# Kernel optimization log

Measured on AMD Instinct MI355X. Metric: run time of the kernel, lower is better.

## Reference

```python
import jax, jax.numpy as jnp
import numpy as np

V = 128          # vocab_size
S = 32           # sentence_size
E = 16           # embedding_size
M = 128          # memory_size
L = 128          # linear_output_size
B = 16
N = 127


def _position_encoding(sentence_size, embedding_size):
    enc = np.ones((embedding_size, sentence_size), dtype=np.float32)
    ls = sentence_size + 1
    le = embedding_size + 1
    for i in range(1, le):
        for j in range(1, ls):
            enc[i - 1, j - 1] = (i - (le - 1) / 2) * (j - (ls - 1) / 2)
    enc = 1 + 4 * enc / embedding_size / sentence_size
    return enc.T  # [S, E]


def setup_inputs() -> dict:
    key = jax.random.key(0)
    ks = jax.random.split(key, 12)
    node_fts = jax.random.randint(ks[0], (B, N, S), 0, V).astype(jnp.float32)
    edge_fts = jax.random.randint(ks[1], (B, N, N, S), 0, V).astype(jnp.float32)
    graph_fts = jax.random.randint(ks[2], (B, S), 0, V).astype(jnp.float32)
    adj_mat = jax.random.randint(ks[3], (B, N, N), 0, 2).astype(jnp.float32)
    hidden = jnp.zeros((B, N, E), jnp.float32)
    sc = 0.02
    query_biases = sc * jax.random.normal(ks[4], (V - 1, E), jnp.float32)
    stories_biases = sc * jax.random.normal(ks[5], (V - 1, E), jnp.float32)
    output_biases = sc * jax.random.normal(ks[6], (V - 1, E), jnp.float32)
    memory_contents = sc * jax.random.normal(ks[7], (M, E), jnp.float32)
    W_int = sc * jax.random.normal(ks[8], (E, E), jnp.float32)   # intermediate_linear (unused, num_hops=1)
    W_out = sc * jax.random.normal(ks[9], (E, L), jnp.float32)   # output_linear
    W_fin = sc * jax.random.normal(ks[10], (L, V), jnp.float32)  # final_linear
    enc = jnp.asarray(_position_encoding(S, E))
    return dict(node_fts=node_fts, edge_fts=edge_fts, graph_fts=graph_fts,
                adj_mat=adj_mat, hidden=hidden, enc=enc,
                query_biases=query_biases, stories_biases=stories_biases,
                output_biases=output_biases, memory_contents=memory_contents,
                W_int=W_int, W_out=W_out, W_fin=W_fin)


def reference(node_fts, edge_fts, graph_fts, adj_mat, hidden, enc,
              query_biases, stories_biases, output_biases, memory_contents,
              W_int, W_out, W_fin):
    del hidden
    b, n, s = node_fts.shape
    # [B, N+1, S]: nodes plus graph feature row
    naf = jnp.concatenate([node_fts, graph_fts[:, None, :]], axis=1)
    # mask edges then pad to [B, N+1, N+1, S]
    ef = edge_fts * adj_mat[..., None]
    ef = jnp.pad(ef, ((0, 0), (0, 1), (0, 1), (0, 0)))
    bt = b * (n + 1)
    queries = naf.reshape(bt, s)                 # [BT, S]
    stories = ef.reshape(bt, n + 1, s)           # [BT, M0, S], M0 = N+1

    nil = jnp.zeros((1, enc.shape[1]), queries.dtype)
    sb = jnp.concatenate([stories_biases, nil], axis=0)   # [V, E]
    qb = jnp.concatenate([query_biases, nil], axis=0)
    ob = jnp.concatenate([output_biases, nil], axis=0)

    sidx = jnp.maximum(stories.astype(jnp.int32), 0)       # clamp_min(0)
    qidx = jnp.maximum(queries.astype(jnp.int32), 0)

    # position-encoded weighted sums over the sentence axis
    mem = jnp.einsum('bmse,se->bme', sb[sidx], enc)        # [BT, M0, E]
    Cj = jnp.einsum('bmse,se->bme', ob[sidx], enc)         # [BT, M0, E]
    pad_m = memory_contents.shape[0] - (n + 1)
    mem = jnp.pad(mem, ((0, 0), (0, pad_m), (0, 0))) + memory_contents
    Cj = jnp.pad(Cj, ((0, 0), (0, pad_m), (0, 0)))
    u = jnp.einsum('bse,se->be', qb[qidx], enc)            # [BT, E]

    # num_hops = 1
    x = u
    probs = jax.nn.softmax(jnp.einsum('bme,be->bm', mem, x), axis=-1)
    o = jnp.einsum('bme,bm->be', Cj, probs)
    x = jax.nn.relu((x + o) @ W_out)                       # last hop -> output_linear + relu
    ret = x @ W_fin                                        # [BT, V]

    nxt = ret.reshape(b, n + 1, -1)
    return nxt[:, :-1, :] + nxt[:, -1:, :]                 # [B, N, V]
```

## Files before the change

kernel.cpp:

```cpp
#include <hip/hip_runtime.h>

#define Vn 128
#define Bn 16
#define Nn 127
#define BTn 2048
#define TRS 20

__device__ __forceinline__ unsigned rneb(float f) {
    unsigned u = __float_as_uint(f);
    return (u + 0x7fffu + ((u >> 16) & 1u)) >> 16;
}
__device__ __forceinline__ float encf(int s, float e7) {
    return fmaf(e7, (float)(s - 15) * 0.0078125f, 1.0f);
}

__global__ __launch_bounds__(256, 4) void memnet_main(
    const float* __restrict__ node_fts, const float* __restrict__ edge_fts,
    const float* __restrict__ graph_fts, const float* __restrict__ adjm,
    const float* __restrict__ qb, const float* __restrict__ sb,
    const float* __restrict__ ob, const float* __restrict__ mc,
    const float* __restrict__ wout, const float* __restrict__ wfin,
    float* __restrict__ ret)
{
    __shared__ __align__(16) unsigned tblL[128 * TRS];
    __shared__ unsigned idxw[8 * 128];
    __shared__ float cjT[16 * 129];
    __shared__ float scoresL[128];
    __shared__ float probsL[128];
    __shared__ float opart[128];
    __shared__ unsigned char actF[128];
    __shared__ __align__(16) float uL[16];
    __shared__ float uoL[16];
    __shared__ __align__(16) float cCL[16];
    __shared__ float xL[128];
    __shared__ float red[8];
    __shared__ float k0L;

    const int t = threadIdx.x;
    const int bt = blockIdx.x;
    const int b = bt >> 7;
    const int i = bt & 127;

    for (int c = t; c < 512; c += 256) {
        int r = c >> 2, q = c & 3;
        float4 s4 = make_float4(0.f, 0.f, 0.f, 0.f);
        float4 o4 = make_float4(0.f, 0.f, 0.f, 0.f);
        if (r < 127) {
            s4 = *(const float4*)&sb[r * 16 + q * 4];
            o4 = *(const float4*)&ob[r * 16 + q * 4];
        }
        uint4 pk;
        pk.x = (rneb(o4.x) << 16) | rneb(s4.x);
        pk.y = (rneb(o4.y) << 16) | rneb(s4.y);
        pk.z = (rneb(o4.z) << 16) | rneb(s4.z);
        pk.w = (rneb(o4.w) << 16) | rneb(s4.w);
        *(uint4*)&tblL[r * TRS + q * 4] = pk;
    }
    if (t < 128) {
        bool a = false;
        if (t < 127 && i < 127) a = (adjm[(b * 127 + i) * 127 + t] != 0.f);
        actF[t] = a ? 1 : 0;
    }
    for (int c = t; c < 1024; c += 256) {
        int m = c >> 3, q = c & 7;
        unsigned packed = 0u;
        if (i < 127 && m < 127) {
            float a = adjm[(b * 127 + i) * 127 + m];
            if (a != 0.f) {
                const float4 v = *(const float4*)&edge_fts[(size_t)(((b * 127 + i) * 127 + m)) * 32 + q * 4];
                packed = (unsigned)(int)v.x | ((unsigned)(int)v.y << 8)
                       | ((unsigned)(int)v.z << 16) | ((unsigned)(int)v.w << 24);
            }
        }
        idxw[q * 128 + m] = packed;
    }
    if (t < 16) {
        const float e7 = (float)(t - 7);
        float es = 0.f, ue = 0.f;
        for (int s = 0; s < 32; s++) {
            float ev = encf(s, e7);
            es += ev;
            float qv = (i < 127) ? node_fts[(b * 127 + i) * 32 + s] : graph_fts[b * 32 + s];
            int qi = (int)qv;
            if (qi < 0) qi = 0;
            float w = (qi < 127) ? qb[qi * 16 + t] : 0.f;
            ue = fmaf(w, ev, ue);
        }
        uL[t] = ue;
        cCL[t] = ob[t] * es;
        float kv = sb[t] * es * ue;
        kv += __shfl_xor(kv, 1); kv += __shfl_xor(kv, 2);
        kv += __shfl_xor(kv, 4); kv += __shfl_xor(kv, 8);
        if (t == 0) k0L = kv;
    }
    __syncthreads();

    const int eg4 = (t & 3) * 4;
    const int md = t >> 2;
    const int m0 = md;
    const int m1 = md + 64;
    const bool a0 = (actF[m0] != 0);
    const bool a1 = (actF[m1] != 0);
    const float ef0 = (float)(eg4 - 7), ef1 = (float)(eg4 - 6);
    const float ef2 = (float)(eg4 - 5), ef3 = (float)(eg4 - 4);

    float4 aM0 = make_float4(0.f, 0.f, 0.f, 0.f);
    float4 aM1 = make_float4(0.f, 0.f, 0.f, 0.f);
    float4 aC0 = make_float4(0.f, 0.f, 0.f, 0.f);
    float4 aC1 = make_float4(0.f, 0.f, 0.f, 0.f);

    if (a0) {
#pragma unroll
        for (int sq = 0; sq < 8; sq++) {
            unsigned w0 = idxw[sq * 128 + m0];
#pragma unroll
            for (int j = 0; j < 4; j++) {
                const int s = sq * 4 + j;
                int ix = (int)((w0 >> (8 * j)) & 0xFF);
                const uint4 pk = *(const uint4*)&tblL[ix * TRS + eg4];
                float e0 = encf(s, ef0), e1 = encf(s, ef1);
                float e2 = encf(s, ef2), e3 = encf(s, ef3);
                aM0.x = fmaf(__uint_as_float(pk.x << 16), e0, aM0.x);
                aC0.x = fmaf(__uint_as_float(pk.x & 0xffff0000u), e0, aC0.x);
                aM0.y = fmaf(__uint_as_float(pk.y << 16), e1, aM0.y);
                aC0.y = fmaf(__uint_as_float(pk.y & 0xffff0000u), e1, aC0.y);
                aM0.z = fmaf(__uint_as_float(pk.z << 16), e2, aM0.z);
                aC0.z = fmaf(__uint_as_float(pk.z & 0xffff0000u), e2, aC0.z);
                aM0.w = fmaf(__uint_as_float(pk.w << 16), e3, aM0.w);
                aC0.w = fmaf(__uint_as_float(pk.w & 0xffff0000u), e3, aC0.w);
            }
        }
    }
    if (a1) {
#pragma unroll
        for (int sq = 0; sq < 8; sq++) {
            unsigned w1 = idxw[sq * 128 + m1];
#pragma unroll
            for (int j = 0; j < 4; j++) {
                const int s = sq * 4 + j;
                int ix = (int)((w1 >> (8 * j)) & 0xFF);
                const uint4 pk = *(const uint4*)&tblL[ix * TRS + eg4];
                float e0 = encf(s, ef0), e1 = encf(s, ef1);
                float e2 = encf(s, ef2), e3 = encf(s, ef3);
                aM1.x = fmaf(__uint_as_float(pk.x << 16), e0, aM1.x);
                aC1.x = fmaf(__uint_as_float(pk.x & 0xffff0000u), e0, aC1.x);
                aM1.y = fmaf(__uint_as_float(pk.y << 16), e1, aM1.y);
                aC1.y = fmaf(__uint_as_float(pk.y & 0xffff0000u), e1, aC1.y);
                aM1.z = fmaf(__uint_as_float(pk.z << 16), e2, aM1.z);
                aC1.z = fmaf(__uint_as_float(pk.z & 0xffff0000u), e2, aC1.z);
                aM1.w = fmaf(__uint_as_float(pk.w << 16), e3, aM1.w);
                aC1.w = fmaf(__uint_as_float(pk.w & 0xffff0000u), e3, aC1.w);
            }
        }
    }

    {
        float4 u4 = *(const float4*)&uL[eg4];
        float4 mc0 = *(const float4*)&mc[m0 * 16 + eg4];
        float4 mc1 = *(const float4*)&mc[m1 * 16 + eg4];
        float p0 = (aM0.x + mc0.x) * u4.x + (aM0.y + mc0.y) * u4.y
                 + (aM0.z + mc0.z) * u4.z + (aM0.w + mc0.w) * u4.w;
        float p1 = (aM1.x + mc1.x) * u4.x + (aM1.y + mc1.y) * u4.y
                 + (aM1.z + mc1.z) * u4.z + (aM1.w + mc1.w) * u4.w;
        p0 += __shfl_xor(p0, 1); p0 += __shfl_xor(p0, 2);
        p1 += __shfl_xor(p1, 1); p1 += __shfl_xor(p1, 2);
        if ((t & 3) == 0) {
            scoresL[m0] = p0 + (a0 ? 0.f : k0L);
            scoresL[m1] = p1 + (a1 ? 0.f : k0L);
        }
        float4 cC4 = *(const float4*)&cCL[eg4];
        float4 c0 = a0 ? aC0 : cC4;
        float4 c1 = a1 ? aC1 : cC4;
        cjT[(eg4 + 0) * 129 + m0] = c0.x; cjT[(eg4 + 1) * 129 + m0] = c0.y;
        cjT[(eg4 + 2) * 129 + m0] = c0.z; cjT[(eg4 + 3) * 129 + m0] = c0.w;
        cjT[(eg4 + 0) * 129 + m1] = c1.x; cjT[(eg4 + 1) * 129 + m1] = c1.y;
        cjT[(eg4 + 2) * 129 + m1] = c1.z; cjT[(eg4 + 3) * 129 + m1] = c1.w;
    }
    __syncthreads();

    {
        float v = (t < 128) ? scoresL[t] : -1e30f;
#pragma unroll
        for (int off = 32; off > 0; off >>= 1) v = fmaxf(v, __shfl_xor(v, off));
        if ((t & 63) == 0) red[t >> 6] = v;
        __syncthreads();
        float mx = fmaxf(fmaxf(red[0], red[1]), fmaxf(red[2], red[3]));
        float ex = (t < 128) ? __expf(scoresL[t] - mx) : 0.f;
        float sv = ex;
#pragma unroll
        for (int off = 32; off > 0; off >>= 1) sv += __shfl_xor(sv, off);
        __syncthreads();
        if ((t & 63) == 0) red[t >> 6] = sv;
        __syncthreads();
        float sum = red[0] + red[1] + red[2] + red[3];
        if (t < 128) probsL[t] = ex / sum;
    }
    __syncthreads();

    if (t < 128) {
        int e = t & 15, ch = t >> 4;
        float acc = 0.f;
#pragma unroll
        for (int k = 0; k < 16; k++) {
            int m = ch * 16 + k;
            acc = fmaf(probsL[m], cjT[e * 129 + m], acc);
        }
        opart[t] = acc;
    }
    __syncthreads();
    if (t < 16) {
        float o = 0.f;
#pragma unroll
        for (int ch = 0; ch < 8; ch++) o += opart[ch * 16 + t];
        uoL[t] = uL[t] + o;
    }
    __syncthreads();

    if (t < 128) {
        float acc = 0.f;
#pragma unroll
        for (int e = 0; e < 16; e++) acc = fmaf(uoL[e], wout[e * 128 + t], acc);
        xL[t] = fmaxf(acc, 0.f);
    }
    __syncthreads();
    if (t < 128) {
        float acc = 0.f;
        for (int l = 0; l < 128; l++) acc = fmaf(xL[l], wfin[l * 128 + t], acc);
        ret[bt * 128 + t] = acc;
    }
}

__global__ void memnet_out(const float* __restrict__ ret, float* __restrict__ out)
{
    int idx = blockIdx.x * 256 + threadIdx.x;
    if (idx >= Bn * Nn * Vn) return;
    int v = idx & 127;
    int r = idx >> 7;
    int b = r / 127;
    int i = r - b * 127;
    out[idx] = ret[(b * 128 + i) * 128 + v] + ret[(b * 128 + 127) * 128 + v];
}

extern "C" void kernel_launch(void* const* d_in, const int* in_sizes, int n_in,
                              void* d_out, int out_size, void* d_ws, size_t ws_size,
                              hipStream_t stream)
{
    const float* node  = (const float*)d_in[0];
    const float* edge  = (const float*)d_in[1];
    const float* graph = (const float*)d_in[2];
    const float* adjm  = (const float*)d_in[3];
    const float* qb    = (const float*)d_in[6];
    const float* sb    = (const float*)d_in[7];
    const float* ob    = (const float*)d_in[8];
    const float* mc    = (const float*)d_in[9];
    const float* wout  = (const float*)d_in[11];
    const float* wfin  = (const float*)d_in[12];

    float* ws = (float*)d_ws;

    memnet_main<<<BTn, 256, 0, stream>>>(node, edge, graph, adjm, qb,
                                         sb, ob, mc, wout, wfin, ws);
    const int total = Bn * Nn * Vn;
    memnet_out<<<(total + 255) / 256, 256, 0, stream>>>(ws, (float*)d_out);
}
```

Baseline: 133.3 us.

## Shrink main kernel to one wavefront with ballot masks and prefetched edge loads

The main kernel now runs each (batch,row) block as a single 64-lane wavefront instead of 256 threads. Adjacency masks come from wave ballots, edge features are loaded straight into registers with a one-step prefetch and redistributed by shuffles rather than staged in shared memory, and softmax and reductions use shuffles with no cross-wave shared buffers. Cj is stored as packed bf16, so the block needs less shared memory and fewer barriers. Each lane now does more serial work over eight memory slots, and rounding Cj to bf16 adds some precision loss.

New measurement: 145.7 us. 9.3% more time.

```diff
diff --git a/kernel.cpp b/kernel.cpp
--- a/kernel.cpp
+++ b/kernel.cpp
@@ -13,8 +13,10 @@
 __device__ __forceinline__ float encf(int s, float e7) {
     return fmaf(e7, (float)(s - 15) * 0.0078125f, 1.0f);
 }
-
-__global__ __launch_bounds__(256, 4) void memnet_main(
+__device__ __forceinline__ float bflo(unsigned p) { return __uint_as_float(p << 16); }
+__device__ __forceinline__ float bfhi(unsigned p) { return __uint_as_float(p & 0xffff0000u); }
+
+__global__ __launch_bounds__(64, 4) void memnet_main(
     const float* __restrict__ node_fts, const float* __restrict__ edge_fts,
     const float* __restrict__ graph_fts, const float* __restrict__ adjm,
     const float* __restrict__ qb, const float* __restrict__ sb,
@@ -23,210 +25,201 @@
     float* __restrict__ ret)
 {
     __shared__ __align__(16) unsigned tblL[128 * TRS];
-    __shared__ unsigned idxw[8 * 128];
-    __shared__ float cjT[16 * 129];
+    __shared__ __align__(8) unsigned cjB[128 * 8];
     __shared__ float scoresL[128];
     __shared__ float probsL[128];
-    __shared__ float opart[128];
-    __shared__ unsigned char actF[128];
     __shared__ __align__(16) float uL[16];
+    __shared__ __align__(16) float cCL[16];
     __shared__ float uoL[16];
-    __shared__ __align__(16) float cCL[16];
     __shared__ float xL[128];
-    __shared__ float red[8];
-    __shared__ float k0L;
-
-    const int t = threadIdx.x;
+
+    const int l  = threadIdx.x;
+    const int q  = l >> 2;
+    const int j4 = l & 3;
+    const int eg4 = j4 * 4;
     const int bt = blockIdx.x;
-    const int b = bt >> 7;
-    const int i = bt & 127;
-
-    for (int c = t; c < 512; c += 256) {
-        int r = c >> 2, q = c & 3;
+    const int b  = bt >> 7;
+    const int i  = bt & 127;
+    const int row = b * 127 + i;
+
+    bool aLo = false, aHi = false;
+    if (i < 127) {
+        aLo = (adjm[row * 127 + l] != 0.f);
+        if (l < 63) aHi = (adjm[row * 127 + 64 + l] != 0.f);
+    }
+    const unsigned long long mk0 = __ballot(aLo);
+    const unsigned long long mk1 = __ballot(aHi);
+
+    float k0;
+    {
+        const int e = l >> 2, g = l & 3;
+        const float e7 = (float)(e - 7);
+        float ue = 0.f;
+#pragma unroll
+        for (int so = 0; so < 8; ++so) {
+            int s = g * 8 + so;
+            float qv = (i < 127) ? node_fts[row * 32 + s] : graph_fts[b * 32 + s];
+            int qi = (int)qv; if (qi < 0) qi = 0;
+            float w = (qi < 127) ? qb[qi * 16 + e] : 0.f;
+            ue = fmaf(w, encf(s, e7), ue);
+        }
+        ue += __shfl_xor(ue, 1); ue += __shfl_xor(ue, 2);
+        const float es = fmaf(e7, 0.125f, 32.f);
+        if (g == 0) { uL[e] = ue; cCL[e] = ob[e] * es; }
+        float kv = (g == 0) ? sb[e] * es * ue : 0.f;
+        kv += __shfl_xor(kv, 1);  kv += __shfl_xor(kv, 2);
+        kv += __shfl_xor(kv, 4);  kv += __shfl_xor(kv, 8);
+        kv += __shfl_xor(kv, 16); kv += __shfl_xor(kv, 32);
+        k0 = kv;
+    }
+
+#pragma unroll
+    for (int k = 0; k < 8; ++k) {
+        int c = l + 64 * k;
+        int r = c >> 2, qd = c & 3;
         float4 s4 = make_float4(0.f, 0.f, 0.f, 0.f);
         float4 o4 = make_float4(0.f, 0.f, 0.f, 0.f);
         if (r < 127) {
-            s4 = *(const float4*)&sb[r * 16 + q * 4];
-            o4 = *(const float4*)&ob[r * 16 + q * 4];
+            s4 = *(const float4*)&sb[r * 16 + qd * 4];
+            o4 = *(const float4*)&ob[r * 16 + qd * 4];
         }
         uint4 pk;
         pk.x = (rneb(o4.x) << 16) | rneb(s4.x);
         pk.y = (rneb(o4.y) << 16) | rneb(s4.y);
         pk.z = (rneb(o4.z) << 16) | rneb(s4.z);
         pk.w = (rneb(o4.w) << 16) | rneb(s4.w);
-        *(uint4*)&tblL[r * TRS + q * 4] = pk;
-    }
-    if (t < 128) {
-        bool a = false;
-        if (t < 127 && i < 127) a = (adjm[(b * 127 + i) * 127 + t] != 0.f);
-        actF[t] = a ? 1 : 0;
-    }
-    for (int c = t; c < 1024; c += 256) {
-        int m = c >> 3, q = c & 7;
-        unsigned packed = 0u;
-        if (i < 127 && m < 127) {
-            float a = adjm[(b * 127 + i) * 127 + m];
-            if (a != 0.f) {
-                const float4 v = *(const float4*)&edge_fts[(size_t)(((b * 127 + i) * 127 + m)) * 32 + q * 4];
-                packed = (unsigned)(int)v.x | ((unsigned)(int)v.y << 8)
-                       | ((unsigned)(int)v.z << 16) | ((unsigned)(int)v.w << 24);
-            }
-        }
-        idxw[q * 128 + m] = packed;
-    }
-    if (t < 16) {
-        const float e7 = (float)(t - 7);
-        float es = 0.f, ue = 0.f;
-        for (int s = 0; s < 32; s++) {
-            float ev = encf(s, e7);
-            es += ev;
-            float qv = (i < 127) ? node_fts[(b * 127 + i) * 32 + s] : graph_fts[b * 32 + s];
-            int qi = (int)qv;
-            if (qi < 0) qi = 0;
-            float w = (qi < 127) ? qb[qi * 16 + t] : 0.f;
-            ue = fmaf(w, ev, ue);
-        }
-        uL[t] = ue;
-        cCL[t] = ob[t] * es;
-        float kv = sb[t] * es * ue;
-        kv += __shfl_xor(kv, 1); kv += __shfl_xor(kv, 2);
-        kv += __shfl_xor(kv, 4); kv += __shfl_xor(kv, 8);
-        if (t == 0) k0L = kv;
-    }
-    __syncthreads();
-
-    const int eg4 = (t & 3) * 4;
-    const int md = t >> 2;
-    const int m0 = md;
-    const int m1 = md + 64;
-    const bool a0 = (actF[m0] != 0);
-    const bool a1 = (actF[m1] != 0);
+        *(uint4*)&tblL[r * TRS + qd * 4] = pk;
+    }
+    __syncthreads();
+
+    const float4 u4  = *(const float4*)&uL[eg4];
+    const float4 cC4 = *(const float4*)&cCL[eg4];
     const float ef0 = (float)(eg4 - 7), ef1 = (float)(eg4 - 6);
     const float ef2 = (float)(eg4 - 5), ef3 = (float)(eg4 - 4);
 
-    float4 aM0 = make_float4(0.f, 0.f, 0.f, 0.f);
-    float4 aM1 = make_float4(0.f, 0.f, 0.f, 0.f);
-    float4 aC0 = make_float4(0.f, 0.f, 0.f, 0.f);
-    float4 aC1 = make_float4(0.f, 0.f, 0.f, 0.f);
-
-    if (a0) {
-#pragma unroll
-        for (int sq = 0; sq < 8; sq++) {
-            unsigned w0 = idxw[sq * 128 + m0];
-#pragma unroll
-            for (int j = 0; j < 4; j++) {
-                const int s = sq * 4 + j;
-                int ix = (int)((w0 >> (8 * j)) & 0xFF);
-                const uint4 pk = *(const uint4*)&tblL[ix * TRS + eg4];
-                float e0 = encf(s, ef0), e1 = encf(s, ef1);
-                float e2 = encf(s, ef2), e3 = encf(s, ef3);
-                aM0.x = fmaf(__uint_as_float(pk.x << 16), e0, aM0.x);
-                aC0.x = fmaf(__uint_as_float(pk.x & 0xffff0000u), e0, aC0.x);
-                aM0.y = fmaf(__uint_as_float(pk.y << 16), e1, aM0.y);
-                aC0.y = fmaf(__uint_as_float(pk.y & 0xffff0000u), e1, aC0.y);
-                aM0.z = fmaf(__uint_as_float(pk.z << 16), e2, aM0.z);
-                aC0.z = fmaf(__uint_as_float(pk.z & 0xffff0000u), e2, aC0.z);
-                aM0.w = fmaf(__uint_as_float(pk.w << 16), e3, aM0.w);
-                aC0.w = fmaf(__uint_as_float(pk.w & 0xffff0000u), e3, aC0.w);
+    float4 nx0 = make_float4(0,0,0,0), nx1 = make_float4(0,0,0,0);
+    bool na;
+    {
+        int m = q;
+        na = (mk0 >> m) & 1ull;
+        if (na) {
+            const float4* ep = (const float4*)&edge_fts[((((size_t)row) * 127 + m) * 32) + j4 * 8];
+            nx0 = ep[0]; nx1 = ep[1];
+        }
+    }
+
+    for (int r = 0; r < 8; ++r) {
+        const int m = r * 16 + q;
+        const bool a = na;
+        const float4 c0 = nx0, c1 = nx1;
+        const float4 mc4 = *(const float4*)&mc[m * 16 + eg4];
+
+        if (r < 7) {
+            int mn = (r + 1) * 16 + q;
+            na = (((r + 1) < 4 ? mk0 : mk1) >> (mn & 63)) & 1ull;
+            if (na) {
+                const float4* ep = (const float4*)&edge_fts[((((size_t)row) * 127 + mn) * 32) + j4 * 8];
+                nx0 = ep[0]; nx1 = ep[1];
             }
         }
-    }
-    if (a1) {
-#pragma unroll
-        for (int sq = 0; sq < 8; sq++) {
-            unsigned w1 = idxw[sq * 128 + m1];
-#pragma unroll
-            for (int j = 0; j < 4; j++) {
-                const int s = sq * 4 + j;
-                int ix = (int)((w1 >> (8 * j)) & 0xFF);
-                const uint4 pk = *(const uint4*)&tblL[ix * TRS + eg4];
-                float e0 = encf(s, ef0), e1 = encf(s, ef1);
-                float e2 = encf(s, ef2), e3 = encf(s, ef3);
-                aM1.x = fmaf(__uint_as_float(pk.x << 16), e0, aM1.x);
-                aC1.x = fmaf(__uint_as_float(pk.x & 0xffff0000u), e0, aC1.x);
-                aM1.y = fmaf(__uint_as_float(pk.y << 16), e1, aM1.y);
-                aC1.y = fmaf(__uint_as_float(pk.y & 0xffff0000u), e1, aC1.y);
-                aM1.z = fmaf(__uint_as_float(pk.z << 16), e2, aM1.z);
-                aC1.z = fmaf(__uint_as_float(pk.z & 0xffff0000u), e2, aC1.z);
-                aM1.w = fmaf(__uint_as_float(pk.w << 16), e3, aM1.w);
-                aC1.w = fmaf(__uint_as_float(pk.w & 0xffff0000u), e3, aC1.w);
-            }
-        }
-    }
-
-    {
-        float4 u4 = *(const float4*)&uL[eg4];
-        float4 mc0 = *(const float4*)&mc[m0 * 16 + eg4];
-        float4 mc1 = *(const float4*)&mc[m1 * 16 + eg4];
-        float p0 = (aM0.x + mc0.x) * u4.x + (aM0.y + mc0.y) * u4.y
-                 + (aM0.z + mc0.z) * u4.z + (aM0.w + mc0.w) * u4.w;
-        float p1 = (aM1.x + mc1.x) * u4.x + (aM1.y + mc1.y) * u4.y
-                 + (aM1.z + mc1.z) * u4.z + (aM1.w + mc1.w) * u4.w;
-        p0 += __shfl_xor(p0, 1); p0 += __shfl_xor(p0, 2);
-        p1 += __shfl_xor(p1, 1); p1 += __shfl_xor(p1, 2);
-        if ((t & 3) == 0) {
-            scoresL[m0] = p0 + (a0 ? 0.f : k0L);
-            scoresL[m1] = p1 + (a1 ? 0.f : k0L);
-        }
-        float4 cC4 = *(const float4*)&cCL[eg4];
-        float4 c0 = a0 ? aC0 : cC4;
-        float4 c1 = a1 ? aC1 : cC4;
-        cjT[(eg4 + 0) * 129 + m0] = c0.x; cjT[(eg4 + 1) * 129 + m0] = c0.y;
-        cjT[(eg4 + 2) * 129 + m0] = c0.z; cjT[(eg4 + 3) * 129 + m0] = c0.w;
-        cjT[(eg4 + 0) * 129 + m1] = c1.x; cjT[(eg4 + 1) * 129 + m1] = c1.y;
-        cjT[(eg4 + 2) * 129 + m1] = c1.z; cjT[(eg4 + 3) * 129 + m1] = c1.w;
-    }
-    __syncthreads();
-
-    {
-        float v = (t < 128) ? scoresL[t] : -1e30f;
-#pragma unroll
-        for (int off = 32; off > 0; off >>= 1) v = fmaxf(v, __shfl_xor(v, off));
-        if ((t & 63) == 0) red[t >> 6] = v;
-        __syncthreads();
-        float mx = fmaxf(fmaxf(red[0], red[1]), fmaxf(red[2], red[3]));
-        float ex = (t < 128) ? __expf(scoresL[t] - mx) : 0.f;
-        float sv = ex;
-#pragma unroll
-        for (int off = 32; off > 0; off >>= 1) sv += __shfl_xor(sv, off);
-        __syncthreads();
-        if ((t & 63) == 0) red[t >> 6] = sv;
-        __syncthreads();
-        float sum = red[0] + red[1] + red[2] + red[3];
-        if (t < 128) probsL[t] = ex / sum;
-    }
-    __syncthreads();
-
-    if (t < 128) {
-        int e = t & 15, ch = t >> 4;
-        float acc = 0.f;
-#pragma unroll
-        for (int k = 0; k < 16; k++) {
-            int m = ch * 16 + k;
-            acc = fmaf(probsL[m], cjT[e * 129 + m], acc);
-        }
-        opart[t] = acc;
-    }
-    __syncthreads();
-    if (t < 16) {
-        float o = 0.f;
-#pragma unroll
-        for (int ch = 0; ch < 8; ch++) o += opart[ch * 16 + t];
-        uoL[t] = uL[t] + o;
-    }
-    __syncthreads();
-
-    if (t < 128) {
-        float acc = 0.f;
-#pragma unroll
-        for (int e = 0; e < 16; e++) acc = fmaf(uoL[e], wout[e * 128 + t], acc);
-        xL[t] = fmaxf(acc, 0.f);
-    }
-    __syncthreads();
-    if (t < 128) {
-        float acc = 0.f;
-        for (int l = 0; l < 128; l++) acc = fmaf(xL[l], wfin[l * 128 + t], acc);
-        ret[bt * 128 + t] = acc;
+
+        float4 aM = make_float4(0,0,0,0), aC = make_float4(0,0,0,0);
+        if (a) {
+            unsigned p0 = (unsigned)(int)c0.x | ((unsigned)(int)c0.y << 8)
+                        | ((unsigned)(int)c0.z << 16) | ((unsigned)(int)c0.w << 24);
+            unsigned p1 = (unsigned)(int)c1.x | ((unsigned)(int)c1.y << 8)
+                        | ((unsigned)(int)c1.z << 16) | ((unsigned)(int)c1.w << 24);
+            unsigned o0 = __shfl_xor(p0, 1), o1 = __shfl_xor(p1, 1);
+            unsigned q0 = (j4 & 1) ? o0 : p0, q1 = (j4 & 1) ? o1 : p1;
+            unsigned q2 = (j4 & 1) ? p0 : o0, q3 = (j4 & 1) ? p1 : o1;
+            unsigned t0 = __shfl_xor(q0, 2), t1 = __shfl_xor(q1, 2);
+            unsigned t2 = __shfl_xor(q2, 2), t3 = __shfl_xor(q3, 2);
+            unsigned w0 = (j4 & 2) ? t0 : q0, w1 = (j4 & 2) ? t1 : q1;
+            unsigned w2 = (j4 & 2) ? t2 : q2, w3 = (j4 & 2) ? t3 : q3;
+            unsigned w4 = (j4 & 2) ? q0 : t0, w5 = (j4 & 2) ? q1 : t1;
+            unsigned w6 = (j4 & 2) ? q2 : t2, w7 = (j4 & 2) ? q3 : t3;
+
+            auto gstep = [&](unsigned wv, int sbase) {
+#pragma unroll
+                for (int j = 0; j < 4; ++j) {
+                    const int s = sbase + j;
+                    int ix = (int)((wv >> (8 * j)) & 0xFF);
+                    const uint4 pk = *(const uint4*)&tblL[ix * TRS + eg4];
+                    float e0 = encf(s, ef0), e1 = encf(s, ef1);
+                    float e2 = encf(s, ef2), e3 = encf(s, ef3);
+                    aM.x = fmaf(bflo(pk.x), e0, aM.x); aC.x = fmaf(bfhi(pk.x), e0, aC.x);
+                    aM.y = fmaf(bflo(pk.y), e1, aM.y); aC.y = fmaf(bfhi(pk.y), e1, aC.y);
+                    aM.z = fmaf(bflo(pk.z), e2, aM.z); aC.z = fmaf(bfhi(pk.z), e2, aC.z);
+                    aM.w = fmaf(bflo(pk.w), e3, aM.w); aC.w = fmaf(bfhi(pk.w), e3, aC.w);
+                }
+            };
+            gstep(w0, 0);  gstep(w1, 4);  gstep(w2, 8);  gstep(w3, 12);
+            gstep(w4, 16); gstep(w5, 20); gstep(w6, 24); gstep(w7, 28);
+        }
+
+        float p = (aM.x + mc4.x) * u4.x + (aM.y + mc4.y) * u4.y
+                + (aM.z + mc4.z) * u4.z + (aM.w + mc4.w) * u4.w;
+        p += __shfl_xor(p, 1); p += __shfl_xor(p, 2);
+        if (j4 == 0) scoresL[m] = p + (a ? 0.f : k0);
+
+        float4 cc = a ? aC : cC4;
+        unsigned d0 = (rneb(cc.y) << 16) | rneb(cc.x);
+        unsigned d1 = (rneb(cc.w) << 16) | rneb(cc.z);
+        *(uint2*)&cjB[m * 8 + j4 * 2] = make_uint2(d0, d1);
+    }
+    __syncthreads();
+
+    {
+        float s0 = scoresL[l], s1 = scoresL[l + 64];
+        float mx = fmaxf(s0, s1);
+#pragma unroll
+        for (int st = 1; st < 64; st <<= 1) mx = fmaxf(mx, __shfl_xor(mx, st));
+        float e0 = __expf(s0 - mx), e1 = __expf(s1 - mx);
+        float sm = e0 + e1;
+#pragma unroll
+        for (int st = 1; st < 64; st <<= 1) sm += __shfl_xor(sm, st);
+        float inv = 1.f / sm;
+        probsL[l] = e0 * inv;
+        probsL[l + 64] = e1 * inv;
+    }
+    __syncthreads();
+
+    {
+        const int e = l & 15, ch = l >> 4;
+        float oa = 0.f;
+#pragma unroll 8
+        for (int k = 0; k < 32; ++k) {
+            int m = ch * 32 + k;
+            unsigned d = cjB[m * 8 + (e >> 1)];
+            float cv = (e & 1) ? bfhi(d) : bflo(d);
+            oa = fmaf(probsL[m], cv, oa);
+        }
+        oa += __shfl_xor(oa, 16); oa += __shfl_xor(oa, 32);
+        if (l < 16) uoL[l] = uL[l] + oa;
+    }
+    __syncthreads();
+
+    {
+        float rx = 0.f, ry = 0.f;
+#pragma unroll
+        for (int e = 0; e < 16; ++e) {
+            float uoe = uoL[e];
+            const float2 w2 = *(const float2*)&wout[e * 128 + 2 * l];
+            rx = fmaf(uoe, w2.x, rx); ry = fmaf(uoe, w2.y, ry);
+        }
+        xL[2 * l]     = fmaxf(rx, 0.f);
+        xL[2 * l + 1] = fmaxf(ry, 0.f);
+    }
+    __syncthreads();
+    {
+        float rx = 0.f, ry = 0.f;
+#pragma unroll 8
+        for (int ll = 0; ll < 128; ++ll) {
+            float xv = xL[ll];
+            const float2 w2 = *(const float2*)&wfin[ll * 128 + 2 * l];
+            rx = fmaf(xv, w2.x, rx); ry = fmaf(xv, w2.y, ry);
+        }
+        *(float2*)&ret[bt * 128 + 2 * l] = make_float2(rx, ry);
     }
 }
 
@@ -258,8 +251,8 @@
 
     float* ws = (float*)d_ws;
 
-    memnet_main<<<BTn, 256, 0, stream>>>(node, edge, graph, adjm, qb,
-                                         sb, ob, mc, wout, wfin, ws);
+    memnet_main<<<BTn, 64, 0, stream>>>(node, edge, graph, adjm, qb,
+                                        sb, ob, mc, wout, wfin, ws);
     const int total = Bn * Nn * Vn;
     memnet_out<<<(total + 255) / 256, 256, 0, stream>>>(ws, (float*)d_out);
 }
```
